# Kernel tuning notes

Hardware: AMD Instinct MI355X
Metric: run time of the kernel (lower is better)

## Reference

```python
import jax, jax.numpy as jnp
import numpy as np

N = 2097152
RES = 512
N_LEVELS = 6  # 512,256,128,64,32,16 (stop at LIGHT_MIN_RES=16)
MIN_ROUGHNESS = 0.08
MAX_ROUGHNESS = 0.5


def _dot(a, b):
    return jnp.sum(a * b, axis=-1, keepdims=True)


def _safe_normalize(x):
    return x / jnp.sqrt(jnp.clip(_dot(x, x), 1e-20, None))


def _reflect(x, n):
    return 2.0 * _dot(x, n) * n - x


def _rgb_to_srgb(x):
    return jnp.where(x <= 0.0031308, 12.92 * x,
                     1.055 * jnp.power(jnp.maximum(x, 0.0031308), 1.0 / 2.4) - 0.055)


def _cube_face_uv(d):
    # OpenGL / nvdiffrast cube-map convention (inverse of util.cube_to_dir)
    x, y, z = d[..., 0], d[..., 1], d[..., 2]
    ax, ay, az = jnp.abs(x), jnp.abs(y), jnp.abs(z)
    is_x = (ax >= ay) & (ax >= az)
    is_y = (~is_x) & (ay >= az)
    face = jnp.where(is_x, jnp.where(x > 0, 0, 1),
           jnp.where(is_y, jnp.where(y > 0, 2, 3),
                           jnp.where(z > 0, 4, 5)))
    ma = jnp.maximum(jnp.where(is_x, ax, jnp.where(is_y, ay, az)), 1e-20)
    u = jnp.where(is_x, jnp.where(x > 0, -z, z),
        jnp.where(is_y, x, jnp.where(z > 0, x, -x)))
    v = jnp.where(is_y, jnp.where(y > 0, z, -z), -y)
    return face, u / ma, v / ma


def _bilinear_gather(tex, face, fx, fy):
    # tex: [6,H,W,C]; face/fx/fy: [N]
    H, W = tex.shape[1], tex.shape[2]
    x0 = jnp.floor(fx); y0 = jnp.floor(fy)
    tx = (fx - x0)[:, None]; ty = (fy - y0)[:, None]
    x0i = jnp.clip(x0.astype(jnp.int32), 0, W - 1)
    x1i = jnp.clip(x0i + 1, 0, W - 1)
    y0i = jnp.clip(y0.astype(jnp.int32), 0, H - 1)
    y1i = jnp.clip(y0i + 1, 0, H - 1)
    c00 = tex[face, y0i, x0i]; c01 = tex[face, y0i, x1i]
    c10 = tex[face, y1i, x0i]; c11 = tex[face, y1i, x1i]
    return (c00 * (1 - tx) + c01 * tx) * (1 - ty) + (c10 * (1 - tx) + c11 * tx) * ty


def _sample_cubemap(tex, dirs):
    H, W = tex.shape[1], tex.shape[2]
    face, u, v = _cube_face_uv(dirs)
    return _bilinear_gather(tex, face, (u * 0.5 + 0.5) * W - 0.5, (v * 0.5 + 0.5) * H - 0.5)


def _sample_cubemap_mip(mips, dirs, level):
    # trilinear: bilinear in each of the two bracketing mip levels + lerp on level
    L = len(mips)
    samples = jnp.stack([_sample_cubemap(m, dirs) for m in mips], axis=0)  # [L,N,C]
    lvl = jnp.clip(level, 0.0, L - 1.0)
    l0 = jnp.floor(lvl).astype(jnp.int32)
    l1 = jnp.minimum(l0 + 1, L - 1)
    f = (lvl - l0.astype(lvl.dtype))[:, None]
    n = jnp.arange(dirs.shape[0])
    return samples[l0, n] * (1 - f) + samples[l1, n] * f


def _sample_lut(lut, uv):
    # lut: [H,W,C]; uv in [0,1], u -> width, v -> height, clamp boundary
    H, W = lut.shape[0], lut.shape[1]
    fx = uv[:, 0] * W - 0.5; fy = uv[:, 1] * H - 0.5
    x0 = jnp.floor(fx); y0 = jnp.floor(fy)
    tx = (fx - x0)[:, None]; ty = (fy - y0)[:, None]
    x0i = jnp.clip(x0.astype(jnp.int32), 0, W - 1); x1i = jnp.clip(x0i + 1, 0, W - 1)
    y0i = jnp.clip(y0.astype(jnp.int32), 0, H - 1); y1i = jnp.clip(y0i + 1, 0, H - 1)
    c00 = lut[y0i, x0i]; c01 = lut[y0i, x1i]; c10 = lut[y1i, x0i]; c11 = lut[y1i, x1i]
    return (c00 * (1 - tx) + c01 * tx) * (1 - ty) + (c10 * (1 - tx) + c11 * tx) * ty


def _get_mip(roughness, n_levels):
    lo = (jnp.clip(roughness, MIN_ROUGHNESS, MAX_ROUGHNESS) - MIN_ROUGHNESS) \
         / (MAX_ROUGHNESS - MIN_ROUGHNESS) * (n_levels - 2)
    hi = (jnp.clip(roughness, MAX_ROUGHNESS, 1.0) - MAX_ROUGHNESS) / (1.0 - MAX_ROUGHNESS) + n_levels - 2
    return jnp.where(roughness < MAX_ROUGHNESS, lo, hi)


def _shade(view_dir, normal, kd, ks, reflect_occ, diffuse_map, mips, fg_lut):
    roughness = ks[:, 1:2]
    metallic = ks[:, 2:3]
    spec_col = (1.0 - metallic) * 0.04 + kd * metallic
    diff_col = kd * (1.0 - metallic)
    reflvec = _safe_normalize(_reflect(view_dir, normal))
    diffuse = jnp.clip(_sample_cubemap(diffuse_map, normal), 0.0, None)
    shaded = diffuse * diff_col * (1.0 - ks[:, 0:1])
    NdotV = jnp.clip(_dot(view_dir, normal), 1e-4, None)
    fg = _sample_lut(fg_lut, jnp.concatenate([NdotV, roughness], axis=-1))
    miplevel = _get_mip(roughness[:, 0], len(mips))
    spec = jnp.clip(_sample_cubemap_mip(mips, reflvec, miplevel), 0.0, None)
    reflectance = spec_col * fg[:, 0:1] + fg[:, 1:2]
    shaded = shaded + spec * reflectance * (1.0 - reflect_occ)
    return _rgb_to_srgb(jnp.clip(shaded, 0.0, 1.0))


def setup_inputs() -> dict:
    key = jax.random.key(0)
    k = jax.random.split(key, 16)
    inp = {
        "view_dir": _safe_normalize(jax.random.normal(k[0], (N, 3), jnp.float32)),
        "normal": _safe_normalize(jax.random.normal(k[1], (N, 3), jnp.float32)),
        "kd": jax.random.uniform(k[2], (N, 3), jnp.float32),
        "ks": jax.random.uniform(k[3], (N, 3), jnp.float32),
        "reflect_occ": jax.random.uniform(k[4], (N, 1), jnp.float32),
    }
    # learned / prefiltered environment light parameters (from build_mips)
    inp["diffuse_map"] = jax.random.uniform(k[5], (6, 16, 16, 3), jnp.float32)
    res = RES
    for i in range(N_LEVELS):
        inp[f"spec{i}"] = jax.random.uniform(k[6 + i], (6, res, res, 3), jnp.float32)
        res //= 2
    inp["fg_lut"] = jax.random.uniform(k[12], (256, 256, 2), jnp.float32)
    return inp


def reference(view_dir, normal, kd, ks, reflect_occ, diffuse_map,
              spec0, spec1, spec2, spec3, spec4, spec5, fg_lut):
    mips = [spec0, spec1, spec2, spec3, spec4, spec5]
    return _shade(view_dir, normal, kd, ks, reflect_occ, diffuse_map, mips, fg_lut)
```

## Files before the change

kernel.cpp:

```cpp
#include <hip/hip_runtime.h>
#include <hip/hip_fp16.h>
#include <math.h>


typedef unsigned int u32;

__device__ __forceinline__ u32 enc9e5(float r, float g, float b) {
    r = fminf(fmaxf(r, 0.f), 65408.f);
    g = fminf(fmaxf(g, 0.f), 65408.f);
    b = fminf(fmaxf(b, 0.f), 65408.f);
    float maxc = fmaxf(r, fmaxf(g, b));
    int e = ((__float_as_int(maxc) >> 23) & 0xff) - 127;
    int exp_p = max(e + 16, 0);
    float rd = __int_as_float((151 - exp_p) << 23);
    int maxm = (int)(maxc * rd + 0.5f);
    if (maxm == 512) { exp_p += 1; rd *= 0.5f; }
    u32 rm = (u32)(r * rd + 0.5f);
    u32 gm = (u32)(g * rd + 0.5f);
    u32 bm = (u32)(b * rd + 0.5f);
    return rm | (gm << 9) | (bm << 18) | ((u32)exp_p << 27);
}

__device__ __forceinline__ void dec9e5_acc(u32 pk, float w, float& r, float& g, float& b) {
    float scale = __int_as_float((int)(((pk >> 27) & 31u) + 103u) << 23) * w;
    r += (float)(pk & 511u) * scale;
    g += (float)((pk >> 9) & 511u) * scale;
    b += (float)((pk >> 18) & 511u) * scale;
}

__device__ __forceinline__ void gather_q9(uint4 q, float tx, float ty,
                                          float& r, float& g, float& b) {
    float w00 = (1.f - tx) * (1.f - ty);
    float w01 = tx * (1.f - ty);
    float w10 = (1.f - tx) * ty;
    float w11 = tx * ty;
    r = 0.f; g = 0.f; b = 0.f;
    dec9e5_acc(q.x, w00, r, g, b);
    dec9e5_acc(q.y, w01, r, g, b);
    dec9e5_acc(q.z, w10, r, g, b);
    dec9e5_acc(q.w, w11, r, g, b);
}

__device__ __forceinline__ float srgb1(float x) {
    float p = 1.055f * __builtin_amdgcn_exp2f(
                  __builtin_amdgcn_logf(fmaxf(x, 0.0031308f)) * (1.0f / 2.4f)) - 0.055f;
    return (x <= 0.0031308f) ? (12.92f * x) : p;
}

__device__ __forceinline__ void cube_face_uv(float dx, float dy, float dz,
                                             int& face, float& u, float& v) {
    float ax = fabsf(dx), ay = fabsf(dy), az = fabsf(dz);
    bool is_x = (ax >= ay) && (ax >= az);
    bool is_y = (!is_x) && (ay >= az);
    face = is_x ? (dx > 0.f ? 0 : 1)
                : (is_y ? (dy > 0.f ? 2 : 3) : (dz > 0.f ? 4 : 5));
    float ma = fmaxf(is_x ? ax : (is_y ? ay : az), 1e-20f);
    float uu = is_x ? (dx > 0.f ? -dz : dz) : (is_y ? dx : (dz > 0.f ? dx : -dx));
    float vv = is_y ? (dy > 0.f ? dz : -dz) : -dy;
    float inv = __builtin_amdgcn_rcpf(ma);
    u = uu * inv;
    v = vv * inv;
}

#define SPEC_TOTAL 2096640
#define DIF_OFF    SPEC_TOTAL
#define LUT_OFF    (SPEC_TOTAL + 1536)
#define ALL_QUADS  (SPEC_TOTAL + 1536 + 65536)
#define N_TILES    8452
#define MAIN_GRID  2048

__device__ __forceinline__ int spec_off(int l) {
    return (1 << 21) - ((1 << 21) >> (2 * l));
}

__device__ __forceinline__ void gld16(const float4* g, float4* l) {
    __builtin_amdgcn_global_load_lds(
        (const __attribute__((address_space(1))) void*)g,
        (__attribute__((address_space(3))) void*)l,
        16, 0, 0);
}

__global__ __launch_bounds__(256)
void repack_tiled(const float* __restrict__ s0, const float* __restrict__ s1,
                  const float* __restrict__ s2, const float* __restrict__ s3,
                  const float* __restrict__ s4, const float* __restrict__ s5,
                  const float* __restrict__ diffuse_map,
                  const float2* __restrict__ lut,
                  uint4* __restrict__ dst)
{
    __shared__ u32 L[289];
    int b = blockIdx.x;
    int tid = threadIdx.x;

    if (b >= 8196) {
        int t = b - 8196;
        int ty0 = (t >> 4) << 4;
        int tx0 = (t & 15) << 4;
        for (int e = tid; e < 289; e += 256) {
            int ey = e / 17, ex = e - ey * 17;
            int gy = min(ty0 + ey, 255), gx = min(tx0 + ex, 255);
            float2 c = lut[(gy << 8) + gx];
            __half2 h = __floats2half2_rn(c.x, c.y);
            L[e] = *reinterpret_cast<u32*>(&h);
        }
        __syncthreads();
        int qx = tid & 15, qy = tid >> 4;
        uint4 qv;
        qv.x = L[qy * 17 + qx];       qv.y = L[qy * 17 + qx + 1];
        qv.z = L[(qy + 1) * 17 + qx]; qv.w = L[(qy + 1) * 17 + qx + 1];
        dst[LUT_OFF + ((ty0 + qy) << 8) + tx0 + qx] = qv;
        return;
    }

    const float* src; int lr, tbase, doff;
    if      (b < 6144) { src = s0; lr = 9; tbase = 0;    doff = 0; }
    else if (b < 7680) { src = s1; lr = 8; tbase = 6144; doff = 1572864; }
    else if (b < 8064) { src = s2; lr = 7; tbase = 7680; doff = 1966080; }
    else if (b < 8160) { src = s3; lr = 6; tbase = 8064; doff = 2064384; }
    else if (b < 8184) { src = s4; lr = 5; tbase = 8160; doff = 2088960; }
    else if (b < 8190) { src = s5; lr = 4; tbase = 8184; doff = 2095104; }
    else               { src = diffuse_map; lr = 4; tbase = 8190; doff = DIF_OFF; }

    int W = 1 << lr;
    int lt = lr - 4;
    int local = b - tbase;
    int face = local >> (2 * lt);
    int rem  = local & ((1 << (2 * lt)) - 1);
    int ty0 = (rem >> lt) << 4;
    int tx0 = (rem & ((1 << lt) - 1)) << 4;
    int fbase = face << (2 * lr);

    for (int e = tid; e < 289; e += 256) {
        int ey = e / 17, ex = e - ey * 17;
        int gy = min(ty0 + ey, W - 1), gx = min(tx0 + ex, W - 1);
        int idx = 3 * (fbase + (gy << lr) + gx);
        L[e] = enc9e5(src[idx], src[idx + 1], src[idx + 2]);
    }
    __syncthreads();
    int qx = tid & 15, qy = tid >> 4;
    uint4 qv;
    qv.x = L[qy * 17 + qx];       qv.y = L[qy * 17 + qx + 1];
    qv.z = L[(qy + 1) * 17 + qx]; qv.w = L[(qy + 1) * 17 + qx + 1];
    dst[doff + fbase + ((ty0 + qy) << lr) + tx0 + qx] = qv;
}

__device__ __forceinline__ void stage_chunk(float* sb, int tid,
    const float* __restrict__ vd, const float* __restrict__ nm,
    const float* __restrict__ kd, const float* __restrict__ ks,
    const float* __restrict__ oc, int base, int nblk)
{
    if (nblk == 256) {
        const float4* v4 = (const float4*)(vd + 3 * base);
        const float4* n4 = (const float4*)(nm + 3 * base);
        const float4* k4 = (const float4*)(kd + 3 * base);
        const float4* q4 = (const float4*)(ks + 3 * base);
        const float4* o4 = (const float4*)(oc + base);
        float4* d4 = (float4*)sb;
        #pragma unroll
        for (int kk = 0; kk < 4; ++kk) {
            int j = tid + (kk << 8);
            if (j < 832) {
                const float4* src; int off;
                if (j < 192)      { src = v4; off = j; }
                else if (j < 384) { src = n4; off = j - 192; }
                else if (j < 576) { src = k4; off = j - 384; }
                else if (j < 768) { src = q4; off = j - 576; }
                else              { src = o4; off = j - 768; }
                gld16(src + off, d4 + j);
            }
        }
    } else {
        for (int j = tid; j < nblk * 3; j += 256) {
            sb[j]        = vd[3 * base + j];
            sb[768 + j]  = nm[3 * base + j];
            sb[1536 + j] = kd[3 * base + j];
            sb[2304 + j] = ks[3 * base + j];
        }
        for (int j = tid; j < nblk; j += 256)
            sb[3072 + j] = oc[base + j];
    }
}

__device__ __forceinline__ void shade_pt(const float* s, int tid,
                                         const uint4* __restrict__ q,
                                         float* __restrict__ outp)
{
    float vx = s[3 * tid], vy = s[3 * tid + 1], vz = s[3 * tid + 2];
    float nx = s[768 + 3 * tid], ny = s[768 + 3 * tid + 1], nz = s[768 + 3 * tid + 2];
    float kdx = s[1536 + 3 * tid], kdy = s[1536 + 3 * tid + 1], kdz = s[1536 + 3 * tid + 2];
    float ks0 = s[2304 + 3 * tid], rough = s[2304 + 3 * tid + 1], metallic = s[2304 + 3 * tid + 2];
    float occ = s[3072 + tid];

    float vdotn = vx * nx + vy * ny + vz * nz;
    float rx = 2.f * vdotn * nx - vx;
    float ry = 2.f * vdotn * ny - vy;
    float rz = 2.f * vdotn * nz - vz;
    float rinv = __builtin_amdgcn_rsqf(fmaxf(rx * rx + ry * ry + rz * rz, 1e-20f));
    rx *= rinv; ry *= rinv; rz *= rinv;

    float dtx, dty; int dIdx;
    {
        int face; float u, v;
        cube_face_uv(nx, ny, nz, face, u, v);
        float fx = (u * 0.5f + 0.5f) * 16.f - 0.5f;
        float fy = (v * 0.5f + 0.5f) * 16.f - 0.5f;
        float x0f = floorf(fx), y0f = floorf(fy);
        dtx = fx - x0f; dty = fy - y0f;
        int x0 = min(max((int)x0f, 0), 15);
        int y0 = min(max((int)y0f, 0), 15);
        dIdx = (face << 8) + (y0 << 4) + x0;
    }

    float ltx, lty; int lutI;
    {
        float NdotV = fmaxf(vdotn, 1e-4f);
        float fx = NdotV * 256.f - 0.5f;
        float fy = rough * 256.f - 0.5f;
        float x0f = floorf(fx), y0f = floorf(fy);
        ltx = fx - x0f; lty = fy - y0f;
        int x0 = min(max((int)x0f, 0), 255);
        int y0 = min(max((int)y0f, 0), 255);
        lutI = (y0 << 8) + x0;
    }

    const float MINR = 0.08f, MAXR = 0.5f;
    float lo = (fminf(fmaxf(rough, MINR), MAXR) - MINR) * (4.0f / (MAXR - MINR));
    float hi = (fminf(fmaxf(rough, MAXR), 1.0f) - MAXR) * (1.0f / (1.0f - MAXR)) + 4.0f;
    float lvl = fminf(fmaxf((rough < MAXR) ? lo : hi, 0.f), 5.f);
    int l0 = min(max((int)floorf(lvl), 0), 5);
    int l1 = min(l0 + 1, 5);
    float fmip = lvl - (float)l0;

    float atx, aty, btx, bty; int aIdx, bIdx;
    {
        int face; float u, v;
        cube_face_uv(rx, ry, rz, face, u, v);
        int lrA = 9 - l0, lrB = 9 - l1;
        float RA = (float)(1 << lrA);
        float fxA = (u * 0.5f + 0.5f) * RA - 0.5f;
        float fyA = (v * 0.5f + 0.5f) * RA - 0.5f;
        float fxB = (l0 == l1) ? fxA : (fxA + 0.5f) * 0.5f - 0.5f;
        float fyB = (l0 == l1) ? fyA : (fyA + 0.5f) * 0.5f - 0.5f;

        float x0fA = floorf(fxA), y0fA = floorf(fyA);
        atx = fxA - x0fA; aty = fyA - y0fA;
        int WA = 1 << lrA;
        int x0A = min(max((int)x0fA, 0), WA - 1);
        int y0A = min(max((int)y0fA, 0), WA - 1);
        aIdx = spec_off(l0) + (face << (2 * lrA)) + (y0A << lrA) + x0A;

        float x0fB = floorf(fxB), y0fB = floorf(fyB);
        btx = fxB - x0fB; bty = fyB - y0fB;
        int WB = 1 << lrB;
        int x0B = min(max((int)x0fB, 0), WB - 1);
        int y0B = min(max((int)y0fB, 0), WB - 1);
        bIdx = spec_off(l1) + (face << (2 * lrB)) + (y0B << lrB) + x0B;
    }

    uint4 qA = q[aIdx];
    uint4 qB = q[bIdx];
    uint4 lq = (q + LUT_OFF)[lutI];
    uint4 dq = (q + DIF_OFF)[dIdx];

    float ar, ag, ab_, br, bg, bb;
    gather_q9(qA, atx, aty, ar, ag, ab_);
    gather_q9(qB, btx, bty, br, bg, bb);

    __half2 h00 = *reinterpret_cast<__half2*>(&lq.x);
    __half2 h01 = *reinterpret_cast<__half2*>(&lq.y);
    __half2 h10 = *reinterpret_cast<__half2*>(&lq.z);
    __half2 h11 = *reinterpret_cast<__half2*>(&lq.w);
    float2 c00 = __half22float2(h00), c01 = __half22float2(h01);
    float2 c10 = __half22float2(h10), c11 = __half22float2(h11);
    float lw00 = (1.f - ltx) * (1.f - lty);
    float lw01 = ltx * (1.f - lty);
    float lw10 = (1.f - ltx) * lty;
    float lw11 = ltx * lty;
    float fg0 = c00.x * lw00 + c01.x * lw01 + c10.x * lw10 + c11.x * lw11;
    float fg1 = c00.y * lw00 + c01.y * lw01 + c10.y * lw10 + c11.y * lw11;

    float dfr, dfg, dfb;
    gather_q9(dq, dtx, dty, dfr, dfg, dfb);
    dfr = fmaxf(dfr, 0.f); dfg = fmaxf(dfg, 0.f); dfb = fmaxf(dfb, 0.f);

    float spr = fmaxf(ar * (1.f - fmip) + br * fmip, 0.f);
    float spg = fmaxf(ag * (1.f - fmip) + bg * fmip, 0.f);
    float spb = fmaxf(ab_ * (1.f - fmip) + bb * fmip, 0.f);

    float m = metallic;
    float scx = (1.f - m) * 0.04f + kdx * m;
    float scy = (1.f - m) * 0.04f + kdy * m;
    float scz = (1.f - m) * 0.04f + kdz * m;
    float dcx = kdx * (1.f - m);
    float dcy = kdy * (1.f - m);
    float dcz = kdz * (1.f - m);

    float kds = 1.f - ks0;
    float om = 1.f - occ;
    float shx = dfr * dcx * kds + spr * (scx * fg0 + fg1) * om;
    float shy = dfg * dcy * kds + spg * (scy * fg0 + fg1) * om;
    float shz = dfb * dcz * kds + spb * (scz * fg0 + fg1) * om;

    outp[0] = srgb1(fminf(fmaxf(shx, 0.f), 1.f));
    outp[1] = srgb1(fminf(fmaxf(shy, 0.f), 1.f));
    outp[2] = srgb1(fminf(fmaxf(shz, 0.f), 1.f));
}

__global__ __launch_bounds__(256, 6)
void envlight_pipe(const float* __restrict__ view_dir,
                   const float* __restrict__ normal,
                   const float* __restrict__ kd,
                   const float* __restrict__ ks,
                   const float* __restrict__ reflect_occ,
                   const uint4* __restrict__ q,
                   float* __restrict__ out, int n)
{
    __shared__ float s_in[2][3328];
    int tid = threadIdx.x;
    int nchunks = (n + 255) >> 8;
    int c = blockIdx.x;
    if (c >= nchunks) return;

    stage_chunk(s_in[0], tid, view_dir, normal, kd, ks, reflect_occ,
                c << 8, min(256, n - (c << 8)));

    int t = 0;
    for (; c < nchunks; c += gridDim.x, ++t) {
        int cur = t & 1;
        __syncthreads();

        int cn = c + gridDim.x;
        if (cn < nchunks)
            stage_chunk(s_in[cur ^ 1], tid, view_dir, normal, kd, ks, reflect_occ,
                        cn << 8, min(256, n - (cn << 8)));

        int base = c << 8;
        int nblk = min(256, n - base);
        if (tid < nblk)
            shade_pt(s_in[cur], tid, q, out + 3 * (base + tid));
    }
}

__global__ __launch_bounds__(256)
void envlight_raw(const float* __restrict__ view_dir,
                  const float* __restrict__ normal,
                  const float* __restrict__ kd,
                  const float* __restrict__ ks,
                  const float* __restrict__ reflect_occ,
                  const float* __restrict__ diffuse_map,
                  const float* __restrict__ s0, const float* __restrict__ s1,
                  const float* __restrict__ s2, const float* __restrict__ s3,
                  const float* __restrict__ s4, const float* __restrict__ s5,
                  const float* __restrict__ fg_lut,
                  float* __restrict__ out, int n)
{
    int i = blockIdx.x * blockDim.x + threadIdx.x;
    if (i >= n) return;

    float vx = view_dir[3 * i], vy = view_dir[3 * i + 1], vz = view_dir[3 * i + 2];
    float nx = normal[3 * i],  ny = normal[3 * i + 1],  nz = normal[3 * i + 2];
    float kdx = kd[3 * i], kdy = kd[3 * i + 1], kdz = kd[3 * i + 2];
    float ks0 = ks[3 * i], rough = ks[3 * i + 1], metallic = ks[3 * i + 2];
    float occ = reflect_occ[i];

    float vdotn = vx * nx + vy * ny + vz * nz;
    float rx = 2.f * vdotn * nx - vx;
    float ry = 2.f * vdotn * ny - vy;
    float rz = 2.f * vdotn * nz - vz;
    float rinv = __builtin_amdgcn_rsqf(fmaxf(rx * rx + ry * ry + rz * rz, 1e-20f));
    rx *= rinv; ry *= rinv; rz *= rinv;

    const float* mips[6] = {s0, s1, s2, s3, s4, s5};

    const float MINR = 0.08f, MAXR = 0.5f;
    float lo = (fminf(fmaxf(rough, MINR), MAXR) - MINR) * (4.0f / (MAXR - MINR));
    float hi = (fminf(fmaxf(rough, MAXR), 1.0f) - MAXR) * (1.0f / (1.0f - MAXR)) + 4.0f;
    float lvl = fminf(fmaxf((rough < MAXR) ? lo : hi, 0.f), 5.f);
    int l0 = min(max((int)floorf(lvl), 0), 5);
    int l1 = min(l0 + 1, 5);
    float f = lvl - (float)l0;

    float acc[3][3];
    float dirs[3][3] = {{nx, ny, nz}, {rx, ry, rz}, {rx, ry, rz}};
    int lrs[3] = {4, 9 - l0, 9 - l1};
    const float* texs[3] = {diffuse_map, mips[l0], mips[l1]};
    for (int s = 0; s < 3; ++s) {
        int face; float u, v;
        cube_face_uv(dirs[s][0], dirs[s][1], dirs[s][2], face, u, v);
        int lr = lrs[s], W = 1 << lr;
        float fx = (u * 0.5f + 0.5f) * (float)W - 0.5f;
        float fy = (v * 0.5f + 0.5f) * (float)W - 0.5f;
        float x0f = floorf(fx), y0f = floorf(fy);
        float tx = fx - x0f, ty = fy - y0f;
        int x0 = min(max((int)x0f, 0), W - 1);
        int x1 = min(x0 + 1, W - 1);
        int y0 = min(max((int)y0f, 0), W - 1);
        int y1 = min(y0 + 1, W - 1);
        int base = face << (2 * lr);
        const float* t = texs[s];
        const float* p00 = t + 3 * (base + (y0 << lr) + x0);
        const float* p01 = t + 3 * (base + (y0 << lr) + x1);
        const float* p10 = t + 3 * (base + (y1 << lr) + x0);
        const float* p11 = t + 3 * (base + (y1 << lr) + x1);
        float w00 = (1.f - tx) * (1.f - ty), w01 = tx * (1.f - ty);
        float w10 = (1.f - tx) * ty, w11 = tx * ty;
        for (int c = 0; c < 3; ++c)
            acc[s][c] = p00[c] * w00 + p01[c] * w01 + p10[c] * w10 + p11[c] * w11;
    }

    float NdotV = fmaxf(vdotn, 1e-4f);
    float fx = NdotV * 256.f - 0.5f, fy = rough * 256.f - 0.5f;
    float x0f = floorf(fx), y0f = floorf(fy);
    float tx = fx - x0f, ty = fy - y0f;
    int x0 = min(max((int)x0f, 0), 255);
    int x1 = min(x0 + 1, 255);
    int y0 = min(max((int)y0f, 0), 255);
    int y1 = min(y0 + 1, 255);
    const float2* lut2 = (const float2*)fg_lut;
    float2 c00 = lut2[(y0 << 8) + x0], c01 = lut2[(y0 << 8) + x1];
    float2 c10 = lut2[(y1 << 8) + x0], c11 = lut2[(y1 << 8) + x1];
    float w00 = (1.f - tx) * (1.f - ty), w01 = tx * (1.f - ty);
    float w10 = (1.f - tx) * ty, w11 = tx * ty;
    float fg0 = c00.x * w00 + c01.x * w01 + c10.x * w10 + c11.x * w11;
    float fg1 = c00.y * w00 + c01.y * w01 + c10.y * w10 + c11.y * w11;

    float dfr = fmaxf(acc[0][0], 0.f), dfg = fmaxf(acc[0][1], 0.f), dfb = fmaxf(acc[0][2], 0.f);
    float spr = fmaxf(acc[1][0] * (1.f - f) + acc[2][0] * f, 0.f);
    float spg = fmaxf(acc[1][1] * (1.f - f) + acc[2][1] * f, 0.f);
    float spb = fmaxf(acc[1][2] * (1.f - f) + acc[2][2] * f, 0.f);

    float m = metallic;
    float scx = (1.f - m) * 0.04f + kdx * m;
    float scy = (1.f - m) * 0.04f + kdy * m;
    float scz = (1.f - m) * 0.04f + kdz * m;
    float kds = 1.f - ks0;
    float om = 1.f - occ;
    float shx = dfr * kdx * (1.f - m) * kds + spr * (scx * fg0 + fg1) * om;
    float shy = dfg * kdy * (1.f - m) * kds + spg * (scy * fg0 + fg1) * om;
    float shz = dfb * kdz * (1.f - m) * kds + spb * (scz * fg0 + fg1) * om;

    out[3 * i + 0] = srgb1(fminf(fmaxf(shx, 0.f), 1.f));
    out[3 * i + 1] = srgb1(fminf(fmaxf(shy, 0.f), 1.f));
    out[3 * i + 2] = srgb1(fminf(fmaxf(shz, 0.f), 1.f));
}

extern "C" void kernel_launch(void* const* d_in, const int* in_sizes, int n_in,
                              void* d_out, int out_size, void* d_ws, size_t ws_size,
                              hipStream_t stream) {
    const float* view_dir    = (const float*)d_in[0];
    const float* normal      = (const float*)d_in[1];
    const float* kd          = (const float*)d_in[2];
    const float* ks          = (const float*)d_in[3];
    const float* reflect_occ = (const float*)d_in[4];
    const float* diffuse_map = (const float*)d_in[5];
    const float* s0          = (const float*)d_in[6];
    const float* s1          = (const float*)d_in[7];
    const float* s2          = (const float*)d_in[8];
    const float* s3          = (const float*)d_in[9];
    const float* s4          = (const float*)d_in[10];
    const float* s5          = (const float*)d_in[11];
    const float* fg_lut      = (const float*)d_in[12];
    float* out = (float*)d_out;

    int n = in_sizes[0] / 3;
    const size_t NEED_Q = (size_t)ALL_QUADS * 16;

    if (ws_size >= NEED_Q) {
        uint4* q = (uint4*)d_ws;
        repack_tiled<<<N_TILES, 256, 0, stream>>>(
            s0, s1, s2, s3, s4, s5, diffuse_map, (const float2*)fg_lut, q);
        int nchunks = (n + 255) >> 8;
        int grid = min(nchunks, MAIN_GRID);
        envlight_pipe<<<grid, 256, 0, stream>>>(
            view_dir, normal, kd, ks, reflect_occ, q, out, n);
    } else {
        int grid = (n + 255) / 256;
        envlight_raw<<<grid, 256, 0, stream>>>(
            view_dir, normal, kd, ks, reflect_occ, diffuse_map,
            s0, s1, s2, s3, s4, s5, fg_lut, out, n);
    }
}
```

Baseline: 228.9 us.

## Replace LDS double-buffered persistent shading kernel with direct per-thread loads

Drops the persistent-grid kernel that staged per-point inputs into shared memory via global_load_lds with double buffering. Each thread now loads its own float3 inputs straight from global memory and writes its output, using one block per 256 points and a launch bound of 8 waves. This removes LDS usage, barriers and staging overhead, which allows higher occupancy. In exchange, the float3 loads are strided and less coalesced, and the explicit prefetch overlap is gone.

```diff
diff --git a/kernel.cpp b/kernel.cpp
--- a/kernel.cpp
+++ b/kernel.cpp
@@ -67,17 +67,9 @@
 #define LUT_OFF    (SPEC_TOTAL + 1536)
 #define ALL_QUADS  (SPEC_TOTAL + 1536 + 65536)
 #define N_TILES    8452
-#define MAIN_GRID  2048
 
 __device__ __forceinline__ int spec_off(int l) {
     return (1 << 21) - ((1 << 21) >> (2 * l));
-}
-
-__device__ __forceinline__ void gld16(const float4* g, float4* l) {
-    __builtin_amdgcn_global_load_lds(
-        (const __attribute__((address_space(1))) void*)g,
-        (__attribute__((address_space(3))) void*)l,
-        16, 0, 0);
 }
 
 __global__ __launch_bounds__(256)
@@ -144,52 +136,28 @@
     dst[doff + fbase + ((ty0 + qy) << lr) + tx0 + qx] = qv;
 }
 
-__device__ __forceinline__ void stage_chunk(float* sb, int tid,
-    const float* __restrict__ vd, const float* __restrict__ nm,
-    const float* __restrict__ kd, const float* __restrict__ ks,
-    const float* __restrict__ oc, int base, int nblk)
+__global__ __launch_bounds__(256, 8)
+void envlight_direct(const float* __restrict__ view_dir,
+                     const float* __restrict__ normal,
+                     const float* __restrict__ kd_p,
+                     const float* __restrict__ ks_p,
+                     const float* __restrict__ reflect_occ,
+                     const uint4* __restrict__ q,
+                     float* __restrict__ out, int n)
 {
-    if (nblk == 256) {
-        const float4* v4 = (const float4*)(vd + 3 * base);
-        const float4* n4 = (const float4*)(nm + 3 * base);
-        const float4* k4 = (const float4*)(kd + 3 * base);
-        const float4* q4 = (const float4*)(ks + 3 * base);
-        const float4* o4 = (const float4*)(oc + base);
-        float4* d4 = (float4*)sb;
-        #pragma unroll
-        for (int kk = 0; kk < 4; ++kk) {
-            int j = tid + (kk << 8);
-            if (j < 832) {
-                const float4* src; int off;
-                if (j < 192)      { src = v4; off = j; }
-                else if (j < 384) { src = n4; off = j - 192; }
-                else if (j < 576) { src = k4; off = j - 384; }
-                else if (j < 768) { src = q4; off = j - 576; }
-                else              { src = o4; off = j - 768; }
-                gld16(src + off, d4 + j);
-            }
-        }
-    } else {
-        for (int j = tid; j < nblk * 3; j += 256) {
-            sb[j]        = vd[3 * base + j];
-            sb[768 + j]  = nm[3 * base + j];
-            sb[1536 + j] = kd[3 * base + j];
-            sb[2304 + j] = ks[3 * base + j];
-        }
-        for (int j = tid; j < nblk; j += 256)
-            sb[3072 + j] = oc[base + j];
-    }
-}
-
-__device__ __forceinline__ void shade_pt(const float* s, int tid,
-                                         const uint4* __restrict__ q,
-                                         float* __restrict__ outp)
-{
-    float vx = s[3 * tid], vy = s[3 * tid + 1], vz = s[3 * tid + 2];
-    float nx = s[768 + 3 * tid], ny = s[768 + 3 * tid + 1], nz = s[768 + 3 * tid + 2];
-    float kdx = s[1536 + 3 * tid], kdy = s[1536 + 3 * tid + 1], kdz = s[1536 + 3 * tid + 2];
-    float ks0 = s[2304 + 3 * tid], rough = s[2304 + 3 * tid + 1], metallic = s[2304 + 3 * tid + 2];
-    float occ = s[3072 + tid];
+    int i = blockIdx.x * blockDim.x + threadIdx.x;
+    if (i >= n) return;
+
+    const float3 v3 = ((const float3*)view_dir)[i];
+    const float3 n3 = ((const float3*)normal)[i];
+    const float3 k3 = ((const float3*)kd_p)[i];
+    const float3 s3 = ((const float3*)ks_p)[i];
+    float occ = reflect_occ[i];
+
+    float vx = v3.x, vy = v3.y, vz = v3.z;
+    float nx = n3.x, ny = n3.y, nz = n3.z;
+    float kdx = k3.x, kdy = k3.y, kdz = k3.z;
+    float ks0 = s3.x, rough = s3.y, metallic = s3.z;
 
     float vdotn = vx * nx + vy * ny + vz * nz;
     float rx = 2.f * vdotn * nx - vx;
@@ -301,44 +269,9 @@
     float shy = dfg * dcy * kds + spg * (scy * fg0 + fg1) * om;
     float shz = dfb * dcz * kds + spb * (scz * fg0 + fg1) * om;
 
-    outp[0] = srgb1(fminf(fmaxf(shx, 0.f), 1.f));
-    outp[1] = srgb1(fminf(fmaxf(shy, 0.f), 1.f));
-    outp[2] = srgb1(fminf(fmaxf(shz, 0.f), 1.f));
-}
-
-__global__ __launch_bounds__(256, 6)
-void envlight_pipe(const float* __restrict__ view_dir,
-                   const float* __restrict__ normal,
-                   const float* __restrict__ kd,
-                   const float* __restrict__ ks,
-                   const float* __restrict__ reflect_occ,
-                   const uint4* __restrict__ q,
-                   float* __restrict__ out, int n)
-{
-    __shared__ float s_in[2][3328];
-    int tid = threadIdx.x;
-    int nchunks = (n + 255) >> 8;
-    int c = blockIdx.x;
-    if (c >= nchunks) return;
-
-    stage_chunk(s_in[0], tid, view_dir, normal, kd, ks, reflect_occ,
-                c << 8, min(256, n - (c << 8)));
-
-    int t = 0;
-    for (; c < nchunks; c += gridDim.x, ++t) {
-        int cur = t & 1;
-        __syncthreads();
-
-        int cn = c + gridDim.x;
-        if (cn < nchunks)
-            stage_chunk(s_in[cur ^ 1], tid, view_dir, normal, kd, ks, reflect_occ,
-                        cn << 8, min(256, n - (cn << 8)));
-
-        int base = c << 8;
-        int nblk = min(256, n - base);
-        if (tid < nblk)
-            shade_pt(s_in[cur], tid, q, out + 3 * (base + tid));
-    }
+    out[3 * i + 0] = srgb1(fminf(fmaxf(shx, 0.f), 1.f));
+    out[3 * i + 1] = srgb1(fminf(fmaxf(shy, 0.f), 1.f));
+    out[3 * i + 2] = srgb1(fminf(fmaxf(shz, 0.f), 1.f));
 }
 
 __global__ __launch_bounds__(256)
@@ -463,19 +396,18 @@
     float* out = (float*)d_out;
 
     int n = in_sizes[0] / 3;
+    int block = 256;
+    int grid = (n + block - 1) / block;
     const size_t NEED_Q = (size_t)ALL_QUADS * 16;
 
     if (ws_size >= NEED_Q) {
         uint4* q = (uint4*)d_ws;
         repack_tiled<<<N_TILES, 256, 0, stream>>>(
             s0, s1, s2, s3, s4, s5, diffuse_map, (const float2*)fg_lut, q);
-        int nchunks = (n + 255) >> 8;
-        int grid = min(nchunks, MAIN_GRID);
-        envlight_pipe<<<grid, 256, 0, stream>>>(
+        envlight_direct<<<grid, block, 0, stream>>>(
             view_dir, normal, kd, ks, reflect_occ, q, out, n);
     } else {
-        int grid = (n + 255) / 256;
-        envlight_raw<<<grid, 256, 0, stream>>>(
+        envlight_raw<<<grid, block, 0, stream>>>(
             view_dir, normal, kd, ks, reflect_occ, diffuse_map,
             s0, s1, s2, s3, s4, s5, fg_lut, out, n);
     }
```

Result: no change. 227.1 us (-0.8%).
